# Optimization experiments

Hardware: AMD Instinct MI355X
Metric: run time of the kernel (lower is better)

## Reference

```python
import jax, jax.numpy as jnp
import numpy as np

B, N, E, DIN, H1, H2, DOUT = 2, 20000, 320000, 128, 256, 256, 128


def setup_inputs() -> dict:
    key = jax.random.key(0)
    ks = jax.random.split(key, 9)
    X = jax.random.normal(ks[0], (B, N, DIN), dtype=jnp.float32)
    edge_index = jax.random.randint(ks[1], (2, E), 0, N, dtype=jnp.int32)
    def lin(k, fan_in, fan_out):
        lim = 1.0 / np.sqrt(fan_in)
        return jax.random.uniform(k, (fan_in, fan_out), jnp.float32, -lim, lim)
    W1 = lin(ks[2], DIN, H1); b1 = jnp.zeros((H1,), jnp.float32)
    W2 = lin(ks[3], H1, H2);  b2 = jnp.zeros((H2,), jnp.float32)
    W3 = lin(ks[4], H2, DOUT); b3 = jnp.zeros((DOUT,), jnp.float32)
    prelu_a = jnp.array(0.25, jnp.float32)  # PReLU default single shared param
    return dict(X=X, W1=W1, b1=b1, W2=W2, b2=b2, W3=W3, b3=b3,
                prelu_a=prelu_a, edge_index=edge_index)


def reference(X, W1, b1, W2, b2, W3, b3, prelu_a, edge_index):
    src, dst = edge_index[0], edge_index[1]
    n = X.shape[1]
    # GCN symmetric normalization with self-loops: deg = in-degree + 1
    deg = jax.ops.segment_sum(jnp.ones_like(src, X.dtype), dst, num_segments=n) + 1.0
    dinv = jax.lax.rsqrt(deg)                      # [N]
    norm_e = dinv[src] * dinv[dst]                 # [E] edge norm
    norm_self = dinv * dinv                        # [N] self-loop norm

    def gcn(x, W, b):
        h = x @ W                                  # [N, F_out]
        agg = jax.ops.segment_sum(h[src] * norm_e[:, None], dst, num_segments=n)
        agg = agg + h * norm_self[:, None]         # add self-loop message
        return agg + b

    def prelu(x):
        return jnp.where(x >= 0, x, prelu_a * x)

    def single(x):  # x: [N, DIN]
        x = prelu(gcn(x, W1, b1))
        x = prelu(gcn(x, W2, b2))
        return gcn(x, W3, b3)

    return jax.vmap(single)(X)                     # [B, N, DOUT]
```

## Files before the change

### kernel.cpp

```cpp
#include <hip/hip_runtime.h>

#define NB 20000
#define EB 320000
#define DIN 128
#define H1D 256
#define H2D 256
#define DOUTD 128


__global__ void zero_kernel(int* __restrict__ p, int n) {
    int t = blockIdx.x * blockDim.x + threadIdx.x;
    if (t < n) p[t] = 0;
}

__global__ void hist_kernel(const int* __restrict__ dst, int* __restrict__ counts) {
    int t = blockIdx.x * blockDim.x + threadIdx.x;
    if (t < EB) atomicAdd(&counts[dst[t]], 1);
}

__global__ __launch_bounds__(1024) void scan_kernel(const int* __restrict__ counts,
                                                    int* __restrict__ row_start,
                                                    int* __restrict__ cursor,
                                                    float* __restrict__ dinv) {
    __shared__ int sums[1024];
    const int CH = (NB + 1023) / 1024;
    int t = threadIdx.x;
    int base = t * CH;
    int s = 0;
    for (int j = 0; j < CH; ++j) {
        int i = base + j;
        if (i < NB) s += counts[i];
    }
    sums[t] = s;
    __syncthreads();
    for (int off = 1; off < 1024; off <<= 1) {
        int v = (t >= off) ? sums[t - off] : 0;
        __syncthreads();
        sums[t] += v;
        __syncthreads();
    }
    int run = sums[t] - s;
    for (int j = 0; j < CH; ++j) {
        int i = base + j;
        if (i < NB) {
            row_start[i] = run;
            cursor[i] = run;
            int c = counts[i];
            run += c;
            dinv[i] = rsqrtf((float)c + 1.0f);
        }
    }
    if (t == 1023) row_start[NB] = sums[1023];
}

__global__ void scatter_kernel(const int* __restrict__ src, const int* __restrict__ dst,
                               const float* __restrict__ dinv,
                               int* __restrict__ cursor, int2* __restrict__ edges) {
    int t = blockIdx.x * blockDim.x + threadIdx.x;
    if (t < EB) {
        int d = dst[t], s = src[t];
        int p = atomicAdd(&cursor[d], 1);
        edges[p] = make_int2(s, __float_as_int(dinv[s] * dinv[d]));
    }
}


__device__ inline void vload(float (&d)[4], const float* p) {
    float4 t = *(const float4*)p; d[0] = t.x; d[1] = t.y; d[2] = t.z; d[3] = t.w;
}
__device__ inline void vload(float (&d)[2], const float* p) {
    float2 t = *(const float2*)p; d[0] = t.x; d[1] = t.y;
}
__device__ inline void vstore(float* p, const float (&d)[4]) {
    *(float4*)p = make_float4(d[0], d[1], d[2], d[3]);
}
__device__ inline void vstore(float* p, const float (&d)[2]) {
    *(float2*)p = make_float2(d[0], d[1]);
}

template <int F, bool BIAS, bool PRELU>
__global__ __launch_bounds__(256) void agg_kernel(
    const float* __restrict__ h, float* __restrict__ out,
    const int* __restrict__ row_start, const int2* __restrict__ edges,
    const float* __restrict__ dinv, const float* __restrict__ bias,
    const float* __restrict__ pa, int nnodes) {
    constexpr int VEC = F / 64;
    int wid = threadIdx.x >> 6;
    int lane = threadIdx.x & 63;
    int g = blockIdx.x * 4 + wid;
    if (g >= nnodes) return;
    int icsr = g;
    int hbase = 0;
    if (icsr >= NB) { icsr -= NB; hbase = NB; }
    const float* hsrc = h + (size_t)hbase * F + (size_t)lane * VEC;
    const float* hown = h + (size_t)g * F + (size_t)lane * VEC;

    float acc0[VEC], acc1[VEC] = {}, acc2[VEC] = {}, acc3[VEC] = {};
    float dv = dinv[icsr];
    float sw = dv * dv;
    {
        float t[VEC];
        vload(t, hown);
#pragma unroll
        for (int v = 0; v < VEC; ++v) acc0[v] = t[v] * sw;
    }
    int e0 = __builtin_amdgcn_readfirstlane(row_start[icsr]);
    int e1 = __builtin_amdgcn_readfirstlane(row_start[icsr + 1]);
    int e = e0;
    for (; e + 4 <= e1; e += 4) {
        int2 ed0 = edges[e], ed1 = edges[e + 1], ed2 = edges[e + 2], ed3 = edges[e + 3];
        float t0[VEC], t1[VEC], t2[VEC], t3[VEC];
        vload(t0, hsrc + (size_t)ed0.x * F);
        vload(t1, hsrc + (size_t)ed1.x * F);
        vload(t2, hsrc + (size_t)ed2.x * F);
        vload(t3, hsrc + (size_t)ed3.x * F);
        float w0 = __int_as_float(ed0.y), w1 = __int_as_float(ed1.y);
        float w2 = __int_as_float(ed2.y), w3 = __int_as_float(ed3.y);
#pragma unroll
        for (int v = 0; v < VEC; ++v) {
            acc0[v] = fmaf(t0[v], w0, acc0[v]);
            acc1[v] = fmaf(t1[v], w1, acc1[v]);
            acc2[v] = fmaf(t2[v], w2, acc2[v]);
            acc3[v] = fmaf(t3[v], w3, acc3[v]);
        }
    }
    for (; e < e1; ++e) {
        int2 ed = edges[e];
        float t[VEC];
        vload(t, hsrc + (size_t)ed.x * F);
        float w = __int_as_float(ed.y);
#pragma unroll
        for (int v = 0; v < VEC; ++v) acc0[v] = fmaf(t[v], w, acc0[v]);
    }
#pragma unroll
    for (int v = 0; v < VEC; ++v) acc0[v] += (acc1[v] + acc2[v]) + acc3[v];
    if (BIAS) {
        float bv[VEC];
        vload(bv, bias + lane * VEC);
#pragma unroll
        for (int v = 0; v < VEC; ++v) acc0[v] += bv[v];
    }
    if (PRELU) {
        float a = *pa;
#pragma unroll
        for (int v = 0; v < VEC; ++v) acc0[v] = acc0[v] >= 0.0f ? acc0[v] : a * acc0[v];
    }
    vstore(out + (size_t)g * F + lane * VEC, acc0);
}

template <bool BIAS, bool PRELU>
__global__ __launch_bounds__(256) void gemm_kernel(const float* __restrict__ A, int M, int K,
                                                   const float* __restrict__ W, int Nc,
                                                   const float* __restrict__ bias,
                                                   const float* __restrict__ pa,
                                                   float* __restrict__ C) {
    __shared__ alignas(16) float As[16][68];
    __shared__ alignas(16) float Bs[16][68];
    int t = threadIdx.x;
    int bm = blockIdx.x * 64;
    int bn = blockIdx.y * 64;
    int tx = t & 15, ty = t >> 4;
    int m0 = ty * 4, n0 = tx * 4;
    int ar = t >> 2, ac4 = (t & 3) * 4;
    int br = t >> 4, bc4 = (t & 15) * 4;

    float acc[4][4] = {};

    for (int k0 = 0; k0 < K; k0 += 16) {
        float4 av = make_float4(0.f, 0.f, 0.f, 0.f);
        int arow = bm + ar;
        if (arow < M) av = *(const float4*)&A[(size_t)arow * K + k0 + ac4];
        As[ac4 + 0][ar] = av.x;
        As[ac4 + 1][ar] = av.y;
        As[ac4 + 2][ar] = av.z;
        As[ac4 + 3][ar] = av.w;
        float4 bv = *(const float4*)&W[(size_t)(k0 + br) * Nc + bn + bc4];
        *(float4*)&Bs[br][bc4] = bv;
        __syncthreads();
#pragma unroll
        for (int k = 0; k < 16; ++k) {
            float4 av4 = *(const float4*)&As[k][m0];
            float4 bv4 = *(const float4*)&Bs[k][n0];
            float a_[4] = {av4.x, av4.y, av4.z, av4.w};
            float b_[4] = {bv4.x, bv4.y, bv4.z, bv4.w};
#pragma unroll
            for (int i = 0; i < 4; ++i)
#pragma unroll
                for (int j = 0; j < 4; ++j)
                    acc[i][j] = fmaf(a_[i], b_[j], acc[i][j]);
        }
        __syncthreads();
    }

    float pav = 0.0f;
    if (PRELU) pav = *pa;
#pragma unroll
    for (int i = 0; i < 4; ++i) {
        int row = bm + m0 + i;
        if (row < M) {
            float v[4];
#pragma unroll
            for (int j = 0; j < 4; ++j) {
                float x = acc[i][j];
                if (BIAS) x += bias[bn + n0 + j];
                if (PRELU) x = (x >= 0.0f) ? x : pav * x;
                v[j] = x;
            }
            *(float4*)&C[(size_t)row * Nc + bn + n0] = make_float4(v[0], v[1], v[2], v[3]);
        }
    }
}


static inline char* carve(char*& p, size_t bytes) {
    char* r = p;
    p += (bytes + 255) & ~(size_t)255;
    return r;
}

extern "C" void kernel_launch(void* const* d_in, const int* in_sizes, int n_in,
                              void* d_out, int out_size, void* d_ws, size_t ws_size,
                              hipStream_t stream) {
    const float* X  = (const float*)d_in[0];
    const float* W1 = (const float*)d_in[1];
    const float* b1 = (const float*)d_in[2];
    const float* W2 = (const float*)d_in[3];
    const float* b2 = (const float*)d_in[4];
    const float* W3 = (const float*)d_in[5];
    const float* b3 = (const float*)d_in[6];
    const float* pa = (const float*)d_in[7];
    const int* ei   = (const int*)d_in[8];
    const int* src = ei;
    const int* dst = ei + EB;
    float* out = (float*)d_out;

    char* p = (char*)d_ws;
    int* counts    = (int*)carve(p, NB * sizeof(int));
    int* row_start = (int*)carve(p, (NB + 1) * sizeof(int));
    int* cursor    = (int*)carve(p, NB * sizeof(int));
    int2* edges    = (int2*)carve(p, EB * sizeof(int2));
    float* dinv    = (float*)carve(p, NB * sizeof(float));

    size_t fixed = (size_t)(p - (char*)d_ws);
    size_t need_fused = fixed + 2 * ((size_t)2 * NB * 256 * sizeof(float) + 256);
    bool fused = ws_size >= need_fused;
    size_t rows = fused ? 2 * NB : NB;
    float* bufA = (float*)carve(p, rows * 256 * sizeof(float));
    float* bufB = (float*)carve(p, rows * 256 * sizeof(float));

    zero_kernel<<<(NB + 255) / 256, 256, 0, stream>>>(counts, NB);
    hist_kernel<<<(EB + 255) / 256, 256, 0, stream>>>(dst, counts);
    scan_kernel<<<1, 1024, 0, stream>>>(counts, row_start, cursor, dinv);
    scatter_kernel<<<(EB + 255) / 256, 256, 0, stream>>>(src, dst, dinv, cursor, edges);

    int nbatch_loops = fused ? 1 : 2;
    for (int b = 0; b < nbatch_loops; ++b) {
        const float* Xb = X + (size_t)b * NB * DIN;
        float* outb = out + (size_t)b * NB * DOUTD;
        int M = (int)rows;
        int aggGrid = (M + 3) / 4;

        agg_kernel<128, false, false><<<aggGrid, 256, 0, stream>>>(
            Xb, bufA, row_start, edges, dinv, nullptr, nullptr, M);
        gemm_kernel<true, true><<<dim3((M + 63) / 64, H1D / 64), 256, 0, stream>>>(
            bufA, M, DIN, W1, H1D, b1, pa, bufB);

        gemm_kernel<false, false><<<dim3((M + 63) / 64, H2D / 64), 256, 0, stream>>>(
            bufB, M, H1D, W2, H2D, nullptr, nullptr, bufA);
        agg_kernel<256, true, true><<<aggGrid, 256, 0, stream>>>(
            bufA, bufB, row_start, edges, dinv, b2, pa, M);

        gemm_kernel<false, false><<<dim3((M + 63) / 64, DOUTD / 64), 256, 0, stream>>>(
            bufB, M, H2D, W3, DOUTD, nullptr, nullptr, bufA);
        agg_kernel<128, true, false><<<aggGrid, 256, 0, stream>>>(
            bufA, outb, row_start, edges, dinv, b3, nullptr, M);
    }
}
```

Baseline: 414.7 us.

## Interleave batches per node in aggregation, enlarge GEMM tile, parallelize CSR scan

Aggregation now handles one node for both batch elements per wave, with each half-wave covering one batch. Intermediates are stored node-interleaved as [N, 2*F], so the CSR edge list and row bounds are read once for both batches and each gathered row is twice as long. The GEMM tile grows from 64 to 128 rows, with 8x4 outputs per thread, to improve register reuse. The single-block 1024-thread scan is replaced by a three-kernel multi-block scan. The fused fallback for small workspaces is removed, so the code now assumes enough workspace for both batches.

```diff
diff --git a/kernel.cpp b/kernel.cpp
--- a/kernel.cpp
+++ b/kernel.cpp
@@ -6,6 +6,7 @@
 #define H1D 256
 #define H2D 256
 #define DOUTD 128
+#define SCAN_BLOCKS ((NB + 255) / 256)
 
 
 __global__ void zero_kernel(int* __restrict__ p, int n) {
@@ -13,44 +14,59 @@
     if (t < n) p[t] = 0;
 }
 
-__global__ void hist_kernel(const int* __restrict__ dst, int* __restrict__ counts) {
+__global__ void hist_kernel(const int* __restrict__ dst, int* __restrict__ bins) {
     int t = blockIdx.x * blockDim.x + threadIdx.x;
-    if (t < EB) atomicAdd(&counts[dst[t]], 1);
-}
-
-__global__ __launch_bounds__(1024) void scan_kernel(const int* __restrict__ counts,
-                                                    int* __restrict__ row_start,
+    if (t < EB) atomicAdd(&bins[dst[t]], 1);
+}
+
+__global__ __launch_bounds__(256) void scanA_kernel(const int* __restrict__ bins,
+                                                    int* __restrict__ loc,
+                                                    int* __restrict__ blksum) {
+    __shared__ int s[256];
+    int t = threadIdx.x;
+    int i = blockIdx.x * 256 + t;
+    int v = (i < NB) ? bins[i] : 0;
+    s[t] = v;
+    __syncthreads();
+    for (int off = 1; off < 256; off <<= 1) {
+        int u = (t >= off) ? s[t - off] : 0;
+        __syncthreads();
+        s[t] += u;
+        __syncthreads();
+    }
+    if (i < NB) loc[i] = s[t] - v;
+    if (t == 255) blksum[blockIdx.x] = s[255];
+}
+
+__global__ __launch_bounds__(128) void scanB_kernel(int* __restrict__ blksum) {
+    __shared__ int s[128];
+    int t = threadIdx.x;
+    int v = (t < SCAN_BLOCKS) ? blksum[t] : 0;
+    s[t] = v;
+    __syncthreads();
+    for (int off = 1; off < 128; off <<= 1) {
+        int u = (t >= off) ? s[t - off] : 0;
+        __syncthreads();
+        s[t] += u;
+        __syncthreads();
+    }
+    if (t < SCAN_BLOCKS) blksum[t] = s[t] - v;
+}
+
+__global__ __launch_bounds__(256) void scanC_kernel(const int* __restrict__ bins,
+                                                    const int* __restrict__ loc,
+                                                    const int* __restrict__ blksum,
+                                                    int* __restrict__ rs,
                                                     int* __restrict__ cursor,
                                                     float* __restrict__ dinv) {
-    __shared__ int sums[1024];
-    const int CH = (NB + 1023) / 1024;
-    int t = threadIdx.x;
-    int base = t * CH;
-    int s = 0;
-    for (int j = 0; j < CH; ++j) {
-        int i = base + j;
-        if (i < NB) s += counts[i];
-    }
-    sums[t] = s;
-    __syncthreads();
-    for (int off = 1; off < 1024; off <<= 1) {
-        int v = (t >= off) ? sums[t - off] : 0;
-        __syncthreads();
-        sums[t] += v;
-        __syncthreads();
-    }
-    int run = sums[t] - s;
-    for (int j = 0; j < CH; ++j) {
-        int i = base + j;
-        if (i < NB) {
-            row_start[i] = run;
-            cursor[i] = run;
-            int c = counts[i];
-            run += c;
-            dinv[i] = rsqrtf((float)c + 1.0f);
-        }
-    }
-    if (t == 1023) row_start[NB] = sums[1023];
+    int i = blockIdx.x * 256 + threadIdx.x;
+    if (i < NB) {
+        int r = loc[i] + blksum[blockIdx.x];
+        rs[i] = r;
+        cursor[i] = r;
+        dinv[i] = rsqrtf((float)bins[i] + 1.0f);
+    }
+    if (i == 0) rs[NB] = EB;
 }
 
 __global__ void scatter_kernel(const int* __restrict__ src, const int* __restrict__ dst,
@@ -65,87 +81,106 @@
 }
 
 
-__device__ inline void vload(float (&d)[4], const float* p) {
-    float4 t = *(const float4*)p; d[0] = t.x; d[1] = t.y; d[2] = t.z; d[3] = t.w;
-}
-__device__ inline void vload(float (&d)[2], const float* p) {
-    float2 t = *(const float2*)p; d[0] = t.x; d[1] = t.y;
-}
-__device__ inline void vstore(float* p, const float (&d)[4]) {
-    *(float4*)p = make_float4(d[0], d[1], d[2], d[3]);
-}
-__device__ inline void vstore(float* p, const float (&d)[2]) {
-    *(float2*)p = make_float2(d[0], d[1]);
-}
-
-template <int F, bool BIAS, bool PRELU>
+template <int NC>
+__device__ inline void ldrow(float4 (&d)[NC], const float* __restrict__ p) {
+#pragma unroll
+    for (int c = 0; c < NC; ++c) d[c] = ((const float4*)p)[c];
+}
+template <int NC>
+__device__ inline void fmarow(float4 (&a)[NC], const float4 (&t)[NC], float w) {
+#pragma unroll
+    for (int c = 0; c < NC; ++c) {
+        a[c].x = fmaf(t[c].x, w, a[c].x);
+        a[c].y = fmaf(t[c].y, w, a[c].y);
+        a[c].z = fmaf(t[c].z, w, a[c].z);
+        a[c].w = fmaf(t[c].w, w, a[c].w);
+    }
+}
+
+template <int F, bool SPLIT_IN, bool SPLIT_OUT, bool BIAS, bool PRELU>
 __global__ __launch_bounds__(256) void agg_kernel(
     const float* __restrict__ h, float* __restrict__ out,
-    const int* __restrict__ row_start, const int2* __restrict__ edges,
+    const int* __restrict__ rs, const int2* __restrict__ edges,
     const float* __restrict__ dinv, const float* __restrict__ bias,
-    const float* __restrict__ pa, int nnodes) {
-    constexpr int VEC = F / 64;
-    int wid = threadIdx.x >> 6;
+    const float* __restrict__ pa) {
+    constexpr int V2 = 2 * F / 64;
+    constexpr int NC = V2 / 4;
+    constexpr int GSTRIDE = SPLIT_IN ? F : 2 * F;
+    int node = blockIdx.x * 4 + (threadIdx.x >> 6);
     int lane = threadIdx.x & 63;
-    int g = blockIdx.x * 4 + wid;
-    if (g >= nnodes) return;
-    int icsr = g;
-    int hbase = 0;
-    if (icsr >= NB) { icsr -= NB; hbase = NB; }
-    const float* hsrc = h + (size_t)hbase * F + (size_t)lane * VEC;
-    const float* hown = h + (size_t)g * F + (size_t)lane * VEC;
-
-    float acc0[VEC], acc1[VEC] = {}, acc2[VEC] = {}, acc3[VEC] = {};
-    float dv = dinv[icsr];
-    float sw = dv * dv;
+    int b = lane >> 5;
+    int fl = (lane & 31) * V2;
+
+    const float* gbase = SPLIT_IN ? (h + (size_t)b * NB * F + fl)
+                                  : (h + (size_t)lane * V2);
+
+    float4 acc0[NC], acc1[NC], acc2[NC], acc3[NC];
     {
-        float t[VEC];
-        vload(t, hown);
-#pragma unroll
-        for (int v = 0; v < VEC; ++v) acc0[v] = t[v] * sw;
-    }
-    int e0 = __builtin_amdgcn_readfirstlane(row_start[icsr]);
-    int e1 = __builtin_amdgcn_readfirstlane(row_start[icsr + 1]);
+        float dv = dinv[node];
+        float sw = dv * dv;
+        float4 tv[NC];
+        ldrow<NC>(tv, gbase + (size_t)node * GSTRIDE);
+#pragma unroll
+        for (int c = 0; c < NC; ++c) {
+            acc0[c] = make_float4(tv[c].x * sw, tv[c].y * sw, tv[c].z * sw, tv[c].w * sw);
+            acc1[c] = make_float4(0.f, 0.f, 0.f, 0.f);
+            acc2[c] = make_float4(0.f, 0.f, 0.f, 0.f);
+            acc3[c] = make_float4(0.f, 0.f, 0.f, 0.f);
+        }
+    }
+
+    int e0 = __builtin_amdgcn_readfirstlane(rs[node]);
+    int e1 = __builtin_amdgcn_readfirstlane(rs[node + 1]);
     int e = e0;
     for (; e + 4 <= e1; e += 4) {
-        int2 ed0 = edges[e], ed1 = edges[e + 1], ed2 = edges[e + 2], ed3 = edges[e + 3];
-        float t0[VEC], t1[VEC], t2[VEC], t3[VEC];
-        vload(t0, hsrc + (size_t)ed0.x * F);
-        vload(t1, hsrc + (size_t)ed1.x * F);
-        vload(t2, hsrc + (size_t)ed2.x * F);
-        vload(t3, hsrc + (size_t)ed3.x * F);
-        float w0 = __int_as_float(ed0.y), w1 = __int_as_float(ed1.y);
-        float w2 = __int_as_float(ed2.y), w3 = __int_as_float(ed3.y);
-#pragma unroll
-        for (int v = 0; v < VEC; ++v) {
-            acc0[v] = fmaf(t0[v], w0, acc0[v]);
-            acc1[v] = fmaf(t1[v], w1, acc1[v]);
-            acc2[v] = fmaf(t2[v], w2, acc2[v]);
-            acc3[v] = fmaf(t3[v], w3, acc3[v]);
-        }
+        int2 d0 = edges[e], d1 = edges[e + 1], d2 = edges[e + 2], d3 = edges[e + 3];
+        float4 t0[NC], t1[NC], t2[NC], t3[NC];
+        ldrow<NC>(t0, gbase + (size_t)d0.x * GSTRIDE);
+        ldrow<NC>(t1, gbase + (size_t)d1.x * GSTRIDE);
+        ldrow<NC>(t2, gbase + (size_t)d2.x * GSTRIDE);
+        ldrow<NC>(t3, gbase + (size_t)d3.x * GSTRIDE);
+        fmarow<NC>(acc0, t0, __int_as_float(d0.y));
+        fmarow<NC>(acc1, t1, __int_as_float(d1.y));
+        fmarow<NC>(acc2, t2, __int_as_float(d2.y));
+        fmarow<NC>(acc3, t3, __int_as_float(d3.y));
     }
     for (; e < e1; ++e) {
-        int2 ed = edges[e];
-        float t[VEC];
-        vload(t, hsrc + (size_t)ed.x * F);
-        float w = __int_as_float(ed.y);
-#pragma unroll
-        for (int v = 0; v < VEC; ++v) acc0[v] = fmaf(t[v], w, acc0[v]);
-    }
-#pragma unroll
-    for (int v = 0; v < VEC; ++v) acc0[v] += (acc1[v] + acc2[v]) + acc3[v];
+        int2 d0 = edges[e];
+        float4 t0[NC];
+        ldrow<NC>(t0, gbase + (size_t)d0.x * GSTRIDE);
+        fmarow<NC>(acc0, t0, __int_as_float(d0.y));
+    }
+
+#pragma unroll
+    for (int c = 0; c < NC; ++c) {
+        acc0[c].x += (acc1[c].x + acc2[c].x) + acc3[c].x;
+        acc0[c].y += (acc1[c].y + acc2[c].y) + acc3[c].y;
+        acc0[c].z += (acc1[c].z + acc2[c].z) + acc3[c].z;
+        acc0[c].w += (acc1[c].w + acc2[c].w) + acc3[c].w;
+    }
     if (BIAS) {
-        float bv[VEC];
-        vload(bv, bias + lane * VEC);
-#pragma unroll
-        for (int v = 0; v < VEC; ++v) acc0[v] += bv[v];
+        float4 bv[NC];
+        ldrow<NC>(bv, bias + fl);
+#pragma unroll
+        for (int c = 0; c < NC; ++c) {
+            acc0[c].x += bv[c].x; acc0[c].y += bv[c].y;
+            acc0[c].z += bv[c].z; acc0[c].w += bv[c].w;
+        }
     }
     if (PRELU) {
         float a = *pa;
 #pragma unroll
-        for (int v = 0; v < VEC; ++v) acc0[v] = acc0[v] >= 0.0f ? acc0[v] : a * acc0[v];
-    }
-    vstore(out + (size_t)g * F + lane * VEC, acc0);
+        for (int c = 0; c < NC; ++c) {
+            acc0[c].x = acc0[c].x >= 0.f ? acc0[c].x : a * acc0[c].x;
+            acc0[c].y = acc0[c].y >= 0.f ? acc0[c].y : a * acc0[c].y;
+            acc0[c].z = acc0[c].z >= 0.f ? acc0[c].z : a * acc0[c].z;
+            acc0[c].w = acc0[c].w >= 0.f ? acc0[c].w : a * acc0[c].w;
+        }
+    }
+    float* obase = SPLIT_OUT ? (out + (size_t)b * NB * F + (size_t)node * F + fl)
+                             : (out + (size_t)node * 2 * F + lane * V2);
+#pragma unroll
+    for (int c = 0; c < NC; ++c) ((float4*)obase)[c] = acc0[c];
 }
 
 template <bool BIAS, bool PRELU>
@@ -154,37 +189,39 @@
                                                    const float* __restrict__ bias,
                                                    const float* __restrict__ pa,
                                                    float* __restrict__ C) {
-    __shared__ alignas(16) float As[16][68];
+    __shared__ alignas(16) float As[16][132];
     __shared__ alignas(16) float Bs[16][68];
     int t = threadIdx.x;
-    int bm = blockIdx.x * 64;
+    int bm = blockIdx.x * 128;
     int bn = blockIdx.y * 64;
     int tx = t & 15, ty = t >> 4;
-    int m0 = ty * 4, n0 = tx * 4;
+    int m0 = ty * 8, n0 = tx * 4;
     int ar = t >> 2, ac4 = (t & 3) * 4;
     int br = t >> 4, bc4 = (t & 15) * 4;
 
-    float acc[4][4] = {};
+    float acc[8][4] = {};
 
     for (int k0 = 0; k0 < K; k0 += 16) {
-        float4 av = make_float4(0.f, 0.f, 0.f, 0.f);
-        int arow = bm + ar;
-        if (arow < M) av = *(const float4*)&A[(size_t)arow * K + k0 + ac4];
-        As[ac4 + 0][ar] = av.x;
-        As[ac4 + 1][ar] = av.y;
-        As[ac4 + 2][ar] = av.z;
-        As[ac4 + 3][ar] = av.w;
+        float4 a0 = make_float4(0.f, 0.f, 0.f, 0.f), a1 = a0;
+        int r0 = bm + ar, r1 = bm + ar + 64;
+        if (r0 < M) a0 = *(const float4*)&A[(size_t)r0 * K + k0 + ac4];
+        if (r1 < M) a1 = *(const float4*)&A[(size_t)r1 * K + k0 + ac4];
+        As[ac4 + 0][ar] = a0.x; As[ac4 + 1][ar] = a0.y;
+        As[ac4 + 2][ar] = a0.z; As[ac4 + 3][ar] = a0.w;
+        As[ac4 + 0][ar + 64] = a1.x; As[ac4 + 1][ar + 64] = a1.y;
+        As[ac4 + 2][ar + 64] = a1.z; As[ac4 + 3][ar + 64] = a1.w;
         float4 bv = *(const float4*)&W[(size_t)(k0 + br) * Nc + bn + bc4];
         *(float4*)&Bs[br][bc4] = bv;
         __syncthreads();
 #pragma unroll
         for (int k = 0; k < 16; ++k) {
-            float4 av4 = *(const float4*)&As[k][m0];
+            float4 av0 = *(const float4*)&As[k][m0];
+            float4 av1 = *(const float4*)&As[k][m0 + 4];
             float4 bv4 = *(const float4*)&Bs[k][n0];
-            float a_[4] = {av4.x, av4.y, av4.z, av4.w};
+            float a_[8] = {av0.x, av0.y, av0.z, av0.w, av1.x, av1.y, av1.z, av1.w};
             float b_[4] = {bv4.x, bv4.y, bv4.z, bv4.w};
 #pragma unroll
-            for (int i = 0; i < 4; ++i)
+            for (int i = 0; i < 8; ++i)
 #pragma unroll
                 for (int j = 0; j < 4; ++j)
                     acc[i][j] = fmaf(a_[i], b_[j], acc[i][j]);
@@ -195,7 +232,7 @@
     float pav = 0.0f;
     if (PRELU) pav = *pa;
 #pragma unroll
-    for (int i = 0; i < 4; ++i) {
+    for (int i = 0; i < 8; ++i) {
         int row = bm + m0 + i;
         if (row < M) {
             float v[4];
@@ -235,44 +272,39 @@
     float* out = (float*)d_out;
 
     char* p = (char*)d_ws;
-    int* counts    = (int*)carve(p, NB * sizeof(int));
-    int* row_start = (int*)carve(p, (NB + 1) * sizeof(int));
-    int* cursor    = (int*)carve(p, NB * sizeof(int));
-    int2* edges    = (int2*)carve(p, EB * sizeof(int2));
-    float* dinv    = (float*)carve(p, NB * sizeof(float));
-
-    size_t fixed = (size_t)(p - (char*)d_ws);
-    size_t need_fused = fixed + 2 * ((size_t)2 * NB * 256 * sizeof(float) + 256);
-    bool fused = ws_size >= need_fused;
-    size_t rows = fused ? 2 * NB : NB;
-    float* bufA = (float*)carve(p, rows * 256 * sizeof(float));
-    float* bufB = (float*)carve(p, rows * 256 * sizeof(float));
-
-    zero_kernel<<<(NB + 255) / 256, 256, 0, stream>>>(counts, NB);
-    hist_kernel<<<(EB + 255) / 256, 256, 0, stream>>>(dst, counts);
-    scan_kernel<<<1, 1024, 0, stream>>>(counts, row_start, cursor, dinv);
+    int* bins    = (int*)carve(p, NB * sizeof(int));
+    int* loc     = (int*)carve(p, NB * sizeof(int));
+    int* blksum  = (int*)carve(p, 128 * sizeof(int));
+    int* rs      = (int*)carve(p, (NB + 1) * sizeof(int));
+    int* cursor  = (int*)carve(p, NB * sizeof(int));
+    int2* edges  = (int2*)carve(p, EB * sizeof(int2));
+    float* dinv  = (float*)carve(p, NB * sizeof(float));
+    float* bufA  = (float*)carve(p, (size_t)2 * NB * 256 * sizeof(float));
+    float* bufB  = (float*)carve(p, (size_t)2 * NB * 256 * sizeof(float));
+
+    const int M = 2 * NB;
+
+    zero_kernel<<<SCAN_BLOCKS, 256, 0, stream>>>(bins, NB);
+    hist_kernel<<<(EB + 255) / 256, 256, 0, stream>>>(dst, bins);
+    scanA_kernel<<<SCAN_BLOCKS, 256, 0, stream>>>(bins, loc, blksum);
+    scanB_kernel<<<1, 128, 0, stream>>>(blksum);
+    scanC_kernel<<<SCAN_BLOCKS, 256, 0, stream>>>(bins, loc, blksum, rs, cursor, dinv);
     scatter_kernel<<<(EB + 255) / 256, 256, 0, stream>>>(src, dst, dinv, cursor, edges);
 
-    int nbatch_loops = fused ? 1 : 2;
-    for (int b = 0; b < nbatch_loops; ++b) {
-        const float* Xb = X + (size_t)b * NB * DIN;
-        float* outb = out + (size_t)b * NB * DOUTD;
-        int M = (int)rows;
-        int aggGrid = (M + 3) / 4;
-
-        agg_kernel<128, false, false><<<aggGrid, 256, 0, stream>>>(
-            Xb, bufA, row_start, edges, dinv, nullptr, nullptr, M);
-        gemm_kernel<true, true><<<dim3((M + 63) / 64, H1D / 64), 256, 0, stream>>>(
-            bufA, M, DIN, W1, H1D, b1, pa, bufB);
-
-        gemm_kernel<false, false><<<dim3((M + 63) / 64, H2D / 64), 256, 0, stream>>>(
-            bufB, M, H1D, W2, H2D, nullptr, nullptr, bufA);
-        agg_kernel<256, true, true><<<aggGrid, 256, 0, stream>>>(
-            bufA, bufB, row_start, edges, dinv, b2, pa, M);
-
-        gemm_kernel<false, false><<<dim3((M + 63) / 64, DOUTD / 64), 256, 0, stream>>>(
-            bufB, M, H2D, W3, DOUTD, nullptr, nullptr, bufA);
-        agg_kernel<128, true, false><<<aggGrid, 256, 0, stream>>>(
-            bufA, outb, row_start, edges, dinv, b3, nullptr, M);
-    }
-}
+    const int aggGrid = NB / 4;
+
+    agg_kernel<128, true, false, false, false><<<aggGrid, 256, 0, stream>>>(
+        X, bufA, rs, edges, dinv, nullptr, nullptr);
+    gemm_kernel<true, true><<<dim3((M + 127) / 128, H1D / 64), 256, 0, stream>>>(
+        bufA, M, DIN, W1, H1D, b1, pa, bufB);
+
+    gemm_kernel<false, false><<<dim3((M + 127) / 128, H2D / 64), 256, 0, stream>>>(
+        bufB, M, H1D, W2, H2D, nullptr, nullptr, bufA);
+    agg_kernel<256, false, false, true, true><<<aggGrid, 256, 0, stream>>>(
+        bufA, bufB, rs, edges, dinv, b2, pa);
+
+    gemm_kernel<false, false><<<dim3((M + 127) / 128, DOUTD / 64), 256, 0, stream>>>(
+        bufB, M, H2D, W3, DOUTD, nullptr, nullptr, bufA);
+    agg_kernel<128, false, true, true, false><<<aggGrid, 256, 0, stream>>>(
+        bufA, out, rs, edges, dinv, b3, nullptr);
+}
```

After: 394.9 us. -4.8%, faster.
